# Optimization experiments

Hardware: AMD Instinct MI355X
Metric: run time of the kernel (lower is better)

Reference implementation:

```python
import jax, jax.numpy as jnp
import numpy as np

N_NODES = 50000
N_EDGES = 800000
IN_CH = 128
HID = 128


def setup_inputs() -> dict:
    key = jax.random.key(0)
    ks = jax.random.split(key, 8)
    s = 0.05
    x = jax.random.normal(ks[0], (N_NODES, IN_CH), dtype=jnp.float32)
    edge_index = jax.random.randint(ks[1], (2, N_EDGES), 0, N_NODES, dtype=jnp.int64)
    W1l = jax.random.normal(ks[2], (IN_CH, HID), dtype=jnp.float32) * s
    W1r = jax.random.normal(ks[3], (IN_CH, HID), dtype=jnp.float32) * s
    b1 = jnp.zeros((HID,), dtype=jnp.float32)
    W2l = jax.random.normal(ks[4], (HID, HID), dtype=jnp.float32) * s
    W2r = jax.random.normal(ks[5], (HID, HID), dtype=jnp.float32) * s
    b2 = jnp.zeros((HID,), dtype=jnp.float32)
    Wout = jax.random.normal(ks[6], (HID, 2), dtype=jnp.float32) * s
    bout = jnp.zeros((2,), dtype=jnp.float32)
    return {"x": x, "edge_index": edge_index, "W1l": W1l, "W1r": W1r, "b1": b1,
            "W2l": W2l, "W2r": W2r, "b2": b2, "Wout": Wout, "bout": bout}


def _mean_aggr(h, src, dst, n_nodes):
    # mean of neighbor (source) features per destination node (PyG SAGEConv default)
    msg_sum = jax.ops.segment_sum(h[src], dst, num_segments=n_nodes)  # [N, D]
    deg = jax.ops.segment_sum(jnp.ones((src.shape[0],), dtype=h.dtype), dst,
                              num_segments=n_nodes)  # [N]
    return msg_sum / jnp.maximum(deg, 1.0)[:, None]


def _sage_conv(h, src, dst, Wl, Wr, b, n_nodes):
    aggr = _mean_aggr(h, src, dst, n_nodes)
    return aggr @ Wl + h @ Wr + b


def reference(x, edge_index, W1l, W1r, b1, W2l, W2r, b2, Wout, bout):
    n = x.shape[0]
    src, dst = edge_index[0], edge_index[1]
    h = jax.nn.relu(_sage_conv(x, src, dst, W1l, W1r, b1, n))
    # dropout is identity in inference mode
    h = jax.nn.relu(_sage_conv(h, src, dst, W2l, W2r, b2, n))
    logits = h @ Wout + bout
    return (logits, h)
```

## Files before the change

kernel.cpp:

```cpp
#include <hip/hip_runtime.h>

#define NN 50000
#define NE 800000
#define CH 128
#define CAP 64
#define NCHUNK ((NE + 255) / 256)
#define EDGE_BLK (NCHUNK * 8)
#define PREP_ITEMS (65536 + NN * (CH / 2))
#define PREP_BLK ((((PREP_ITEMS + 255) / 256) + 7) & ~7)

typedef __attribute__((ext_vector_type(8))) short short8;
typedef __attribute__((ext_vector_type(4))) float float4a;

#define DEG_OFF  0
#define CSR_OFF  50048
#define XB_OFF   1650048
#define AGB_OFF  4850048
#define H1B_OFF  8050048
#define WTP_OFF  11250048

static __device__ __forceinline__ unsigned short f2b(float f) {
    unsigned u = __float_as_uint(f);
    unsigned r = u + 0x7fff + ((u >> 16) & 1);
    return (unsigned short)(r >> 16);
}

__global__ __launch_bounds__(256) void k_build(
    const int* __restrict__ eidx, int* __restrict__ deg,
    unsigned short* __restrict__ csr,
    const float* __restrict__ W1l, const float* __restrict__ W1r,
    const float* __restrict__ W2l, const float* __restrict__ W2r,
    unsigned short* __restrict__ wtp,
    const float* __restrict__ x, unsigned* __restrict__ xb) {
    int b = blockIdx.x;
    if (b >= PREP_BLK) {
        int eb = b - PREP_BLK;
        int p = eb & 7;
        int e = (eb >> 3) * 256 + threadIdx.x;
        if (e < NE) {
            int dst = __builtin_nontemporal_load(eidx + NE + e);
            if ((unsigned)dst < NN && (dst & 7) == p) {
                int src = __builtin_nontemporal_load(eidx + e);
                if ((unsigned)src < NN) {
                    int r = atomicAdd(&deg[dst], 1);
                    r = min(r, CAP - 1);
                    csr[(size_t)dst * CAP + r] = (unsigned short)src;
                }
            }
        }
    } else {
        int i = b * 256 + threadIdx.x;
        if (i < 65536) {
            int layer = i >> 15;
            int li = i & 32767;
            int e = li & 7, lane = (li >> 3) & 63, j = (li >> 9) & 7, kt = li >> 12;
            int ln = lane & 15, quad = lane >> 4;
            int n = j * 16 + ln;
            int k = kt * 32 + quad * 8 + e;
            const float* Wl = layer ? W2l : W1l;
            const float* Wr = layer ? W2r : W1r;
            float v = (k < 128) ? Wl[k * 128 + n] : Wr[(k - 128) * 128 + n];
            wtp[(size_t)layer * 32768 + li] = f2b(v);
        } else if (i < PREP_ITEMS) {
            int i2 = i - 65536;
            unsigned long long pr =
                __builtin_nontemporal_load((const unsigned long long*)x + i2);
            float lo = __uint_as_float((unsigned)pr);
            float hi = __uint_as_float((unsigned)(pr >> 32));
            unsigned pk = (unsigned)f2b(lo) | ((unsigned)f2b(hi) << 16);
            __builtin_nontemporal_store(pk, &xb[i2]);
        }
    }
}

static __device__ __forceinline__ void acc8(float* acc, uint4 v) {
    acc[0] += __uint_as_float(v.x << 16); acc[1] += __uint_as_float(v.x & 0xffff0000u);
    acc[2] += __uint_as_float(v.y << 16); acc[3] += __uint_as_float(v.y & 0xffff0000u);
    acc[4] += __uint_as_float(v.z << 16); acc[5] += __uint_as_float(v.z & 0xffff0000u);
    acc[6] += __uint_as_float(v.w << 16); acc[7] += __uint_as_float(v.w & 0xffff0000u);
}

__global__ __launch_bounds__(256) void k_gather4(
    const int* __restrict__ deg, const unsigned short* __restrict__ csr,
    const uint4* __restrict__ featb, uint4* __restrict__ aggrb) {
    int wave = (blockIdx.x * 256 + threadIdx.x) >> 6;
    int lane = threadIdx.x & 63;
    if (wave >= NN) return;
    int d = min(deg[wave], CAP);
    const unsigned short* row = csr + (size_t)wave * CAP;
    int g = lane >> 4;
    int c = lane & 15;

    float acc[8];
    #pragma unroll
    for (int e = 0; e < 8; ++e) acc[e] = 0.0f;

    int i0 = 0;
    for (; i0 + 16 <= d; i0 += 16) {
        int s1 = row[i0 + g];
        int s2 = row[i0 + 4 + g];
        int s3 = row[i0 + 8 + g];
        int s4 = row[i0 + 12 + g];
        uint4 v1 = featb[(size_t)s1 * 16 + c];
        uint4 v2 = featb[(size_t)s2 * 16 + c];
        uint4 v3 = featb[(size_t)s3 * 16 + c];
        uint4 v4 = featb[(size_t)s4 * 16 + c];
        acc8(acc, v1); acc8(acc, v2); acc8(acc, v3); acc8(acc, v4);
    }
    for (; i0 + 8 <= d; i0 += 8) {
        int s1 = row[i0 + g];
        int s2 = row[i0 + 4 + g];
        uint4 v1 = featb[(size_t)s1 * 16 + c];
        uint4 v2 = featb[(size_t)s2 * 16 + c];
        acc8(acc, v1); acc8(acc, v2);
    }
    if (i0 < d) {
        int n1 = i0 + g, n2 = i0 + 4 + g;
        int s1 = (n1 < d) ? (int)row[n1] : 0;
        int s2 = (n2 < d) ? (int)row[n2] : 0;
        uint4 v1 = featb[(size_t)s1 * 16 + c];
        uint4 v2 = featb[(size_t)s2 * 16 + c];
        if (n1 < d) acc8(acc, v1);
        if (n2 < d) acc8(acc, v2);
    }

    #pragma unroll
    for (int e = 0; e < 8; ++e) {
        acc[e] += __shfl_xor(acc[e], 32, 64);
        acc[e] += __shfl_xor(acc[e], 16, 64);
    }
    if (lane < 16) {
        float s = 1.0f / (float)(d > 1 ? d : 1);
        uint4 o;
        o.x = (unsigned)f2b(acc[0] * s) | ((unsigned)f2b(acc[1] * s) << 16);
        o.y = (unsigned)f2b(acc[2] * s) | ((unsigned)f2b(acc[3] * s) << 16);
        o.z = (unsigned)f2b(acc[4] * s) | ((unsigned)f2b(acc[5] * s) << 16);
        o.w = (unsigned)f2b(acc[6] * s) | ((unsigned)f2b(acc[7] * s) << 16);
        aggrb[(size_t)wave * 16 + c] = o;
    }
}

template <bool BF16OUT>
__global__ __launch_bounds__(256) void k_layer_mfma(
    const short* __restrict__ aggrb, const short* __restrict__ hinb,
    const short* __restrict__ wtp, const float* __restrict__ bias,
    float* __restrict__ outf, unsigned short* __restrict__ outb,
    const float* __restrict__ Wout, const float* __restrict__ bout,
    float* __restrict__ logits) {
    int lane = threadIdx.x & 63;
    int wid = threadIdx.x >> 6;
    int m0 = blockIdx.x * 64 + wid * 16;
    int ln = lane & 15;
    int quad = lane >> 4;
    int mc = min(m0 + ln, NN - 1);

    float4a acc[8];
    #pragma unroll
    for (int j = 0; j < 8; ++j) acc[j] = (float4a){0.0f, 0.0f, 0.0f, 0.0f};

    #pragma unroll
    for (int kt = 0; kt < 8; ++kt) {
        const short* arow = (kt < 4 ? aggrb : hinb) + (size_t)mc * CH + (kt & 3) * 32 + quad * 8;
        short8 av = *(const short8*)arow;
        const short* bk = wtp + (size_t)kt * 4096 + lane * 8;
        #pragma unroll
        for (int j = 0; j < 8; ++j) {
            short8 bv = *(const short8*)(bk + j * 512);
            acc[j] = __builtin_amdgcn_mfma_f32_16x16x32_bf16(av, bv, acc[j], 0, 0, 0);
        }
    }

    float p0[4], p1[4];
    #pragma unroll
    for (int r = 0; r < 4; ++r) { p0[r] = 0.0f; p1[r] = 0.0f; }

    #pragma unroll
    for (int j = 0; j < 8; ++j) {
        int col = j * 16 + ln;
        float bj = bias[col];
        float w0 = 0.0f, w1 = 0.0f;
        if (!BF16OUT) { w0 = Wout[col * 2]; w1 = Wout[col * 2 + 1]; }
        #pragma unroll
        for (int r = 0; r < 4; ++r) {
            int row = m0 + quad * 4 + r;
            float v = fmaxf(acc[j][r] + bj, 0.0f);
            if (row < NN) {
                if (BF16OUT) outb[(size_t)row * CH + col] = f2b(v);
                else         __builtin_nontemporal_store(v, &outf[(size_t)row * CH + col]);
            }
            if (!BF16OUT) { p0[r] = fmaf(v, w0, p0[r]); p1[r] = fmaf(v, w1, p1[r]); }
        }
    }

    if (!BF16OUT) {
        #pragma unroll
        for (int r = 0; r < 4; ++r) {
            #pragma unroll
            for (int off = 1; off < 16; off <<= 1) {
                p0[r] += __shfl_xor(p0[r], off, 64);
                p1[r] += __shfl_xor(p1[r], off, 64);
            }
        }
        if (ln == 0) {
            float b0 = bout[0], b1 = bout[1];
            #pragma unroll
            for (int r = 0; r < 4; ++r) {
                int row = m0 + quad * 4 + r;
                if (row < NN) {
                    logits[row * 2 + 0] = p0[r] + b0;
                    logits[row * 2 + 1] = p1[r] + b1;
                }
            }
        }
    }
}

extern "C" void kernel_launch(void* const* d_in, const int* in_sizes, int n_in,
                              void* d_out, int out_size, void* d_ws, size_t ws_size,
                              hipStream_t stream) {
    const float* x    = (const float*)d_in[0];
    const int*   eidx = (const int*)d_in[1];
    const float* W1l  = (const float*)d_in[2];
    const float* W1r  = (const float*)d_in[3];
    const float* b1   = (const float*)d_in[4];
    const float* W2l  = (const float*)d_in[5];
    const float* W2r  = (const float*)d_in[6];
    const float* b2   = (const float*)d_in[7];
    const float* Wout = (const float*)d_in[8];
    const float* bout = (const float*)d_in[9];

    float* out    = (float*)d_out;
    float* ws     = (float*)d_ws;
    int*   deg    = (int*)ws;
    unsigned short* csr = (unsigned short*)(ws + CSR_OFF);
    unsigned* xb  = (unsigned*)(ws + XB_OFF);
    unsigned* agb = (unsigned*)(ws + AGB_OFF);
    unsigned* h1b = (unsigned*)(ws + H1B_OFF);
    unsigned short* wtp = (unsigned short*)(ws + WTP_OFF);
    float* logits = out;
    float* hout   = out + 100000;

    (void)hipMemsetAsync(deg, 0, NN * sizeof(int), stream);

    k_build<<<PREP_BLK + EDGE_BLK, 256, 0, stream>>>(eidx, deg, csr,
                                                     W1l, W1r, W2l, W2r, wtp, x, xb);

    k_gather4<<<(NN + 3) / 4, 256, 0, stream>>>(deg, csr, (const uint4*)xb, (uint4*)agb);
    k_layer_mfma<true><<<(NN + 63) / 64, 256, 0, stream>>>(
        (const short*)agb, (const short*)xb, (const short*)wtp, b1,
        nullptr, (unsigned short*)h1b, nullptr, nullptr, nullptr);

    k_gather4<<<(NN + 3) / 4, 256, 0, stream>>>(deg, csr, (const uint4*)h1b, (uint4*)agb);
    k_layer_mfma<false><<<(NN + 63) / 64, 256, 0, stream>>>(
        (const short*)agb, (const short*)h1b, (const short*)(wtp + 32768), b2,
        hout, nullptr, Wout, bout, logits);
}
```

Measured before the change: 234.8 us.

## Gather neighbor features from FP8 copies instead of BF16

Adds FP8 copies of the input features and the layer-1 hidden features, and the neighbor-mean gather reads those instead of BF16. This halves the bytes per random gather. CSR indices are now loaded once per wave and broadcast with shuffles. The cost is an extra FP8 write in the prep and layer-1 kernels, plus a real accuracy loss in the aggregated features from FP8 quantization, which may threaten tolerance.

New measurement: 235.3 us. Within noise of the previous version (+0.2%).

```diff
diff --git a/kernel.cpp b/kernel.cpp
--- a/kernel.cpp
+++ b/kernel.cpp
@@ -6,18 +6,21 @@
 #define CAP 64
 #define NCHUNK ((NE + 255) / 256)
 #define EDGE_BLK (NCHUNK * 8)
-#define PREP_ITEMS (65536 + NN * (CH / 2))
+#define PREP_ITEMS (65536 + NN * 32)
 #define PREP_BLK ((((PREP_ITEMS + 255) / 256) + 7) & ~7)
 
 typedef __attribute__((ext_vector_type(8))) short short8;
 typedef __attribute__((ext_vector_type(4))) float float4a;
+typedef __attribute__((ext_vector_type(2))) float vfloat2;
 
 #define DEG_OFF  0
 #define CSR_OFF  50048
 #define XB_OFF   1650048
-#define AGB_OFF  4850048
-#define H1B_OFF  8050048
-#define WTP_OFF  11250048
+#define X8_OFF   4850048
+#define H1B_OFF  6450048
+#define H18_OFF  9650048
+#define AGB_OFF  11250048
+#define WTP_OFF  14450048
 
 static __device__ __forceinline__ unsigned short f2b(float f) {
     unsigned u = __float_as_uint(f);
@@ -31,21 +34,19 @@
     const float* __restrict__ W1l, const float* __restrict__ W1r,
     const float* __restrict__ W2l, const float* __restrict__ W2r,
     unsigned short* __restrict__ wtp,
-    const float* __restrict__ x, unsigned* __restrict__ xb) {
+    const float* __restrict__ x, unsigned* __restrict__ xb, unsigned* __restrict__ x8) {
     int b = blockIdx.x;
     if (b >= PREP_BLK) {
         int eb = b - PREP_BLK;
         int p = eb & 7;
         int e = (eb >> 3) * 256 + threadIdx.x;
         if (e < NE) {
-            int dst = __builtin_nontemporal_load(eidx + NE + e);
-            if ((unsigned)dst < NN && (dst & 7) == p) {
-                int src = __builtin_nontemporal_load(eidx + e);
-                if ((unsigned)src < NN) {
-                    int r = atomicAdd(&deg[dst], 1);
-                    r = min(r, CAP - 1);
-                    csr[(size_t)dst * CAP + r] = (unsigned short)src;
-                }
+            int src = eidx[e];
+            int dst = eidx[NE + e];
+            if ((unsigned)src < NN && (unsigned)dst < NN && (dst & 7) == p) {
+                int r = atomicAdd(&deg[dst], 1);
+                r = min(r, CAP - 1);
+                csr[(size_t)dst * CAP + r] = (unsigned short)src;
             }
         }
     } else {
@@ -63,80 +64,89 @@
             wtp[(size_t)layer * 32768 + li] = f2b(v);
         } else if (i < PREP_ITEMS) {
             int i2 = i - 65536;
-            unsigned long long pr =
-                __builtin_nontemporal_load((const unsigned long long*)x + i2);
-            float lo = __uint_as_float((unsigned)pr);
-            float hi = __uint_as_float((unsigned)(pr >> 32));
-            unsigned pk = (unsigned)f2b(lo) | ((unsigned)f2b(hi) << 16);
-            __builtin_nontemporal_store(pk, &xb[i2]);
-        }
-    }
-}
-
-static __device__ __forceinline__ void acc8(float* acc, uint4 v) {
-    acc[0] += __uint_as_float(v.x << 16); acc[1] += __uint_as_float(v.x & 0xffff0000u);
-    acc[2] += __uint_as_float(v.y << 16); acc[3] += __uint_as_float(v.y & 0xffff0000u);
-    acc[4] += __uint_as_float(v.z << 16); acc[5] += __uint_as_float(v.z & 0xffff0000u);
-    acc[6] += __uint_as_float(v.w << 16); acc[7] += __uint_as_float(v.w & 0xffff0000u);
-}
-
-__global__ __launch_bounds__(256) void k_gather4(
+            unsigned long long p0 = __builtin_nontemporal_load((const unsigned long long*)x + 2 * i2);
+            unsigned long long p1 = __builtin_nontemporal_load((const unsigned long long*)x + 2 * i2 + 1);
+            float f0 = __uint_as_float((unsigned)p0);
+            float f1 = __uint_as_float((unsigned)(p0 >> 32));
+            float f2 = __uint_as_float((unsigned)p1);
+            float f3 = __uint_as_float((unsigned)(p1 >> 32));
+            uint2 bfp;
+            bfp.x = (unsigned)f2b(f0) | ((unsigned)f2b(f1) << 16);
+            bfp.y = (unsigned)f2b(f2) | ((unsigned)f2b(f3) << 16);
+            ((uint2*)xb)[i2] = bfp;
+            int r8 = __builtin_amdgcn_cvt_pk_fp8_f32(f0, f1, 0, false);
+            r8 = __builtin_amdgcn_cvt_pk_fp8_f32(f2, f3, r8, true);
+            x8[i2] = (unsigned)r8;
+        }
+    }
+}
+
+static __device__ __forceinline__ void accf8(float* a, uint4 v) {
+    unsigned u[4] = {v.x, v.y, v.z, v.w};
+    #pragma unroll
+    for (int q = 0; q < 4; ++q) {
+        vfloat2 f0 = __builtin_amdgcn_cvt_pk_f32_fp8((int)u[q], false);
+        vfloat2 f1 = __builtin_amdgcn_cvt_pk_f32_fp8((int)u[q], true);
+        a[q * 4 + 0] += f0[0]; a[q * 4 + 1] += f0[1];
+        a[q * 4 + 2] += f1[0]; a[q * 4 + 3] += f1[1];
+    }
+}
+
+__global__ __launch_bounds__(256) void k_gather8(
     const int* __restrict__ deg, const unsigned short* __restrict__ csr,
-    const uint4* __restrict__ featb, uint4* __restrict__ aggrb) {
+    const uint4* __restrict__ feat8, uint4* __restrict__ aggrb) {
     int wave = (blockIdx.x * 256 + threadIdx.x) >> 6;
     int lane = threadIdx.x & 63;
     if (wave >= NN) return;
     int d = min(deg[wave], CAP);
-    const unsigned short* row = csr + (size_t)wave * CAP;
-    int g = lane >> 4;
-    int c = lane & 15;
-
-    float acc[8];
-    #pragma unroll
-    for (int e = 0; e < 8; ++e) acc[e] = 0.0f;
+    int idx_l = (int)csr[(size_t)wave * CAP + lane];
+    int g = lane >> 3;
+    int c = lane & 7;
+
+    float acc[16];
+    #pragma unroll
+    for (int e = 0; e < 16; ++e) acc[e] = 0.0f;
 
     int i0 = 0;
     for (; i0 + 16 <= d; i0 += 16) {
-        int s1 = row[i0 + g];
-        int s2 = row[i0 + 4 + g];
-        int s3 = row[i0 + 8 + g];
-        int s4 = row[i0 + 12 + g];
-        uint4 v1 = featb[(size_t)s1 * 16 + c];
-        uint4 v2 = featb[(size_t)s2 * 16 + c];
-        uint4 v3 = featb[(size_t)s3 * 16 + c];
-        uint4 v4 = featb[(size_t)s4 * 16 + c];
-        acc8(acc, v1); acc8(acc, v2); acc8(acc, v3); acc8(acc, v4);
-    }
-    for (; i0 + 8 <= d; i0 += 8) {
-        int s1 = row[i0 + g];
-        int s2 = row[i0 + 4 + g];
-        uint4 v1 = featb[(size_t)s1 * 16 + c];
-        uint4 v2 = featb[(size_t)s2 * 16 + c];
-        acc8(acc, v1); acc8(acc, v2);
+        int s1 = __shfl(idx_l, i0 + g, 64);
+        int s2 = __shfl(idx_l, i0 + 8 + g, 64);
+        uint4 v1 = feat8[(size_t)s1 * 8 + c];
+        uint4 v2 = feat8[(size_t)s2 * 8 + c];
+        accf8(acc, v1); accf8(acc, v2);
+    }
+    if (i0 + 8 <= d) {
+        int s1 = __shfl(idx_l, i0 + g, 64);
+        uint4 v1 = feat8[(size_t)s1 * 8 + c];
+        accf8(acc, v1);
+        i0 += 8;
     }
     if (i0 < d) {
-        int n1 = i0 + g, n2 = i0 + 4 + g;
-        int s1 = (n1 < d) ? (int)row[n1] : 0;
-        int s2 = (n2 < d) ? (int)row[n2] : 0;
-        uint4 v1 = featb[(size_t)s1 * 16 + c];
-        uint4 v2 = featb[(size_t)s2 * 16 + c];
-        if (n1 < d) acc8(acc, v1);
-        if (n2 < d) acc8(acc, v2);
-    }
-
-    #pragma unroll
-    for (int e = 0; e < 8; ++e) {
+        int n = i0 + g;
+        int s1 = __shfl(idx_l, (n < d) ? n : 0, 64);
+        uint4 v1 = feat8[(size_t)s1 * 8 + c];
+        if (n < d) accf8(acc, v1);
+    }
+
+    #pragma unroll
+    for (int e = 0; e < 16; ++e) {
         acc[e] += __shfl_xor(acc[e], 32, 64);
         acc[e] += __shfl_xor(acc[e], 16, 64);
-    }
-    if (lane < 16) {
+        acc[e] += __shfl_xor(acc[e], 8, 64);
+    }
+    if (lane < 8) {
         float s = 1.0f / (float)(d > 1 ? d : 1);
-        uint4 o;
-        o.x = (unsigned)f2b(acc[0] * s) | ((unsigned)f2b(acc[1] * s) << 16);
-        o.y = (unsigned)f2b(acc[2] * s) | ((unsigned)f2b(acc[3] * s) << 16);
-        o.z = (unsigned)f2b(acc[4] * s) | ((unsigned)f2b(acc[5] * s) << 16);
-        o.w = (unsigned)f2b(acc[6] * s) | ((unsigned)f2b(acc[7] * s) << 16);
-        aggrb[(size_t)wave * 16 + c] = o;
+        uint4 o1, o2;
+        o1.x = (unsigned)f2b(acc[0] * s)  | ((unsigned)f2b(acc[1] * s)  << 16);
+        o1.y = (unsigned)f2b(acc[2] * s)  | ((unsigned)f2b(acc[3] * s)  << 16);
+        o1.z = (unsigned)f2b(acc[4] * s)  | ((unsigned)f2b(acc[5] * s)  << 16);
+        o1.w = (unsigned)f2b(acc[6] * s)  | ((unsigned)f2b(acc[7] * s)  << 16);
+        o2.x = (unsigned)f2b(acc[8] * s)  | ((unsigned)f2b(acc[9] * s)  << 16);
+        o2.y = (unsigned)f2b(acc[10] * s) | ((unsigned)f2b(acc[11] * s) << 16);
+        o2.z = (unsigned)f2b(acc[12] * s) | ((unsigned)f2b(acc[13] * s) << 16);
+        o2.w = (unsigned)f2b(acc[14] * s) | ((unsigned)f2b(acc[15] * s) << 16);
+        aggrb[(size_t)wave * 16 + 2 * lane] = o1;
+        aggrb[(size_t)wave * 16 + 2 * lane + 1] = o2;
     }
 }
 
@@ -145,6 +155,7 @@
     const short* __restrict__ aggrb, const short* __restrict__ hinb,
     const short* __restrict__ wtp, const float* __restrict__ bias,
     float* __restrict__ outf, unsigned short* __restrict__ outb,
+    unsigned char* __restrict__ out8,
     const float* __restrict__ Wout, const float* __restrict__ bout,
     float* __restrict__ logits) {
     int lane = threadIdx.x & 63;
@@ -185,8 +196,13 @@
             int row = m0 + quad * 4 + r;
             float v = fmaxf(acc[j][r] + bj, 0.0f);
             if (row < NN) {
-                if (BF16OUT) outb[(size_t)row * CH + col] = f2b(v);
-                else         __builtin_nontemporal_store(v, &outf[(size_t)row * CH + col]);
+                if (BF16OUT) {
+                    outb[(size_t)row * CH + col] = f2b(v);
+                    int b8 = __builtin_amdgcn_cvt_pk_fp8_f32(v, v, 0, false);
+                    out8[(size_t)row * CH + col] = (unsigned char)(b8 & 0xff);
+                } else {
+                    __builtin_nontemporal_store(v, &outf[(size_t)row * CH + col]);
+                }
             }
             if (!BF16OUT) { p0[r] = fmaf(v, w0, p0[r]); p1[r] = fmaf(v, w1, p1[r]); }
         }
@@ -234,8 +250,10 @@
     int*   deg    = (int*)ws;
     unsigned short* csr = (unsigned short*)(ws + CSR_OFF);
     unsigned* xb  = (unsigned*)(ws + XB_OFF);
+    unsigned* x8  = (unsigned*)(ws + X8_OFF);
+    unsigned* h1b = (unsigned*)(ws + H1B_OFF);
+    unsigned* h18 = (unsigned*)(ws + H18_OFF);
     unsigned* agb = (unsigned*)(ws + AGB_OFF);
-    unsigned* h1b = (unsigned*)(ws + H1B_OFF);
     unsigned short* wtp = (unsigned short*)(ws + WTP_OFF);
     float* logits = out;
     float* hout   = out + 100000;
@@ -243,15 +261,15 @@
     (void)hipMemsetAsync(deg, 0, NN * sizeof(int), stream);
 
     k_build<<<PREP_BLK + EDGE_BLK, 256, 0, stream>>>(eidx, deg, csr,
-                                                     W1l, W1r, W2l, W2r, wtp, x, xb);
-
-    k_gather4<<<(NN + 3) / 4, 256, 0, stream>>>(deg, csr, (const uint4*)xb, (uint4*)agb);
+                                                     W1l, W1r, W2l, W2r, wtp, x, xb, x8);
+
+    k_gather8<<<(NN + 3) / 4, 256, 0, stream>>>(deg, csr, (const uint4*)x8, (uint4*)agb);
     k_layer_mfma<true><<<(NN + 63) / 64, 256, 0, stream>>>(
         (const short*)agb, (const short*)xb, (const short*)wtp, b1,
-        nullptr, (unsigned short*)h1b, nullptr, nullptr, nullptr);
-
-    k_gather4<<<(NN + 3) / 4, 256, 0, stream>>>(deg, csr, (const uint4*)h1b, (uint4*)agb);
+        nullptr, (unsigned short*)h1b, (unsigned char*)h18, nullptr, nullptr, nullptr);
+
+    k_gather8<<<(NN + 3) / 4, 256, 0, stream>>>(deg, csr, (const uint4*)h18, (uint4*)agb);
     k_layer_mfma<false><<<(NN + 63) / 64, 256, 0, stream>>>(
         (const short*)agb, (const short*)h1b, (const short*)(wtp + 32768), b2,
-        hout, nullptr, Wout, bout, logits);
-}
+        hout, nullptr, nullptr, Wout, bout, logits);
+}
```
